# Kernel optimization log

Hardware: AMD Instinct MI355X
Metric: run time of the kernel (lower is better)

The kernel has to match this reference:

```python
import jax, jax.numpy as jnp
import numpy as np

NUM_POINTS = 500_000
DIM = 3
WINDOW = 64  # 4**DIM cubic B-spline stencil
INV_CELL = 20.0
ORIGIN = (0.0, 0.0, 0.0)


def setup_inputs() -> dict:
    key = jax.random.key(0)
    # particle positions in the interior of the unit cube
    position_stack = jax.random.uniform(
        key, (NUM_POINTS, DIM), dtype=jnp.float32, minval=0.1, maxval=0.9
    )
    return {"position_stack": position_stack}


def _middle_splines(x, h):
    """Cubic B-spline basis and gradient ('middle_splines' branch; the source's
    lax.switch uses index=0 unconditionally). x = dist in grid units, shape [...]."""
    c1 = (x >= -2) & (x < -1)
    c2 = (x >= -1) & (x < 0)
    c3 = (x >= 0) & (x < 1)
    c4 = (x >= 1) & (x < 2)
    basis = jnp.select(
        [c1, c2, c3, c4],
        [
            ((1.0 / 6.0 * x + 1.0) * x + 2.0) * x + 4.0 / 3.0,
            (-0.5 * x - 1.0) * x * x + 2.0 / 3.0,
            (0.5 * x - 1.0) * x * x + 2.0 / 3.0,
            ((-1.0 / 6.0 * x + 1.0) * x - 2.0) * x + 4.0 / 3.0,
        ],
        0.0,
    )
    dbasis = jnp.select(
        [c1, c2, c3, c4],
        [
            h * ((0.5 * x + 2.0) * x + 2.0),
            h * (-1.5 * x - 2.0) * x,
            h * (1.5 * x - 2.0) * x,
            h * ((-0.5 * x + 2.0) * x - 2.0),
        ],
        0.0,
    )
    return basis, dbasis


def _forward(position_stack):
    origin = jnp.asarray(ORIGIN, dtype=position_stack.dtype)
    rel = (position_stack - origin) * INV_CELL            # [N, 3] in grid units
    base = jnp.floor(rel) - 1.0                           # lower corner of 4^3 stencil
    ar = jnp.arange(4, dtype=position_stack.dtype)
    offs = jnp.stack(jnp.meshgrid(ar, ar, ar, indexing="ij"), axis=-1).reshape(-1, DIM)  # [64, 3]
    dist = rel[:, None, :] - (base[:, None, :] + offs[None, :, :])  # [N, 64, 3], in [-2, 2)
    b, db = _middle_splines(dist, INV_CELL)
    shapef_stack = jnp.prod(b, axis=-1)                   # [N, 64]
    shapef_grad_stack = jnp.stack(
        [
            db[..., 0] * b[..., 1] * b[..., 2],
            db[..., 1] * b[..., 0] * b[..., 2],
            db[..., 2] * b[..., 0] * b[..., 1],
        ],
        axis=-1,
    )                                                     # [N, 64, 3]
    return shapef_stack, shapef_grad_stack


def reference(position_stack):
    return _forward(position_stack)
```

## Files before the change

### kernel.cpp

```cpp
#include <hip/hip_runtime.h>

#ifndef INV_CELL_H
#define INV_CELL_H 20.0f
#endif

__device__ __forceinline__ void spline_eval(float f, float g, int idx,
                                            float& b, float& db) {
    float u  = (idx & 1) ? f : g;
    float u2 = u * u;
    float u3 = u2 * u;
    bool outer = (idx == 0) || (idx == 3);
    float b_out = u3 * (1.0f / 6.0f);
    float b_in  = fmaf(0.5f, u3, fmaf(-1.0f, u2, 2.0f / 3.0f));
    b = outer ? b_out : b_in;
    float m_out = 0.5f * u2;
    float m_in  = u * fmaf(-1.5f, u, 2.0f);
    float mag = outer ? m_out : m_in;
    float sgn = (idx >= 2) ? INV_CELL_H : -INV_CELL_H;
    db = mag * sgn;
}

struct F3 { float x, y, z; };

__global__ void __launch_bounds__(256)
cubic_shapefn_kernel(const float* __restrict__ pos,
                     float* __restrict__ shapef,
                     float* __restrict__ grad,
                     int N) {
    int wave = blockIdx.x * 4 + (threadIdx.x >> 6);
    if (wave >= N) return;
    int lane = threadIdx.x & 63;

    float px = pos[(size_t)wave * 3 + 0];
    float py = pos[(size_t)wave * 3 + 1];
    float pz = pos[(size_t)wave * 3 + 2];

    float rx = px * INV_CELL_H, ry = py * INV_CELL_H, rz = pz * INV_CELL_H;
    float fx = rx - floorf(rx), fy = ry - floorf(ry), fz = rz - floorf(rz);
    float gx = 1.0f - fx,       gy = 1.0f - fy,       gz = 1.0f - fz;

    int i = (lane >> 4) & 3;
    int j = (lane >> 2) & 3;
    int k = lane & 3;

    float bx, dbx, by, dby, bz, dbz;
    spline_eval(fx, gx, i, bx, dbx);
    spline_eval(fy, gy, j, by, dby);
    spline_eval(fz, gz, k, bz, dbz);

    float pyz = by * bz;
    float s   = bx * pyz;
    float gxv = dbx * pyz;
    float gyv = dby * (bx * bz);
    float gzv = dbz * (bx * by);

    shapef[(size_t)wave * 64 + lane] = s;

    F3 v{gxv, gyv, gzv};
    *(F3*)(grad + (size_t)wave * 192 + (size_t)lane * 3) = v;
}

extern "C" void kernel_launch(void* const* d_in, const int* in_sizes, int n_in,
                              void* d_out, int out_size, void* d_ws, size_t ws_size,
                              hipStream_t stream) {
    const float* pos = (const float*)d_in[0];
    int N = in_sizes[0] / 3;
    float* shapef = (float*)d_out;
    float* grad   = shapef + (size_t)N * 64;
    int blocks = (N + 3) / 4;
    cubic_shapefn_kernel<<<blocks, 256, 0, stream>>>(pos, shapef, grad, N);
}
```

Baseline: 536.4 us.

## Map 16 threads per point with vectorized nontemporal stores and grid-stride loop

Each point is now handled by 16 threads instead of 64. Each thread computes four z-stencil entries and writes them with 128-bit nontemporal stores instead of scalar and 12-byte stores. The launch becomes a persistent grid-stride loop capped at 2048 blocks, with occupancy hints in launch_bounds. This targets the write-bandwidth-bound output, reducing store instruction count and cache pollution, at the cost of more registers and less parallelism per point.

```diff
diff --git a/kernel.cpp b/kernel.cpp
--- a/kernel.cpp
+++ b/kernel.cpp
@@ -3,6 +3,8 @@
 #ifndef INV_CELL_H
 #define INV_CELL_H 20.0f
 #endif
+
+typedef float f32x4 __attribute__((ext_vector_type(4)));
 
 __device__ __forceinline__ void spline_eval(float f, float g, int idx,
                                             float& b, float& db) {
@@ -20,44 +22,57 @@
     db = mag * sgn;
 }
 
-struct F3 { float x, y, z; };
-
-__global__ void __launch_bounds__(256)
+__global__ void __launch_bounds__(256, 8)
 cubic_shapefn_kernel(const float* __restrict__ pos,
                      float* __restrict__ shapef,
                      float* __restrict__ grad,
                      int N) {
-    int wave = blockIdx.x * 4 + (threadIdx.x >> 6);
-    if (wave >= N) return;
-    int lane = threadIdx.x & 63;
+    const int t = threadIdx.x & 15;
+    const int i = t >> 2;
+    const int j = t & 3;
+    const int group0  = (int)((blockIdx.x * blockDim.x + threadIdx.x) >> 4);
+    const int ngroups = (int)((gridDim.x * blockDim.x) >> 4);
 
-    float px = pos[(size_t)wave * 3 + 0];
-    float py = pos[(size_t)wave * 3 + 1];
-    float pz = pos[(size_t)wave * 3 + 2];
+    for (int p = group0; p < N; p += ngroups) {
+        float px = pos[(size_t)p * 3 + 0];
+        float py = pos[(size_t)p * 3 + 1];
+        float pz = pos[(size_t)p * 3 + 2];
 
-    float rx = px * INV_CELL_H, ry = py * INV_CELL_H, rz = pz * INV_CELL_H;
-    float fx = rx - floorf(rx), fy = ry - floorf(ry), fz = rz - floorf(rz);
-    float gx = 1.0f - fx,       gy = 1.0f - fy,       gz = 1.0f - fz;
+        float rx = px * INV_CELL_H, ry = py * INV_CELL_H, rz = pz * INV_CELL_H;
+        float fx = rx - floorf(rx), fy = ry - floorf(ry), fz = rz - floorf(rz);
+        float gx = 1.0f - fx,       gy = 1.0f - fy,       gz = 1.0f - fz;
 
-    int i = (lane >> 4) & 3;
-    int j = (lane >> 2) & 3;
-    int k = lane & 3;
+        float bx, dbx, by, dby;
+        spline_eval(fx, gx, i, bx, dbx);
+        spline_eval(fy, gy, j, by, dby);
 
-    float bx, dbx, by, dby, bz, dbz;
-    spline_eval(fx, gx, i, bx, dbx);
-    spline_eval(fy, gy, j, by, dby);
-    spline_eval(fz, gz, k, bz, dbz);
+        float bz[4], dbz[4];
+#pragma unroll
+        for (int k = 0; k < 4; ++k) spline_eval(fz, gz, k, bz[k], dbz[k]);
 
-    float pyz = by * bz;
-    float s   = bx * pyz;
-    float gxv = dbx * pyz;
-    float gyv = dby * (bx * bz);
-    float gzv = dbz * (bx * by);
+        float A  = bx * by;
+        float Bx = dbx * by;
+        float By = bx * dby;
 
-    shapef[(size_t)wave * 64 + lane] = s;
+        f32x4 sv = { A * bz[0], A * bz[1], A * bz[2], A * bz[3] };
 
-    F3 v{gxv, gyv, gzv};
-    *(F3*)(grad + (size_t)wave * 192 + (size_t)lane * 3) = v;
+        float gxk[4], gyk[4], gzk[4];
+#pragma unroll
+        for (int k = 0; k < 4; ++k) {
+            gxk[k] = Bx * bz[k];
+            gyk[k] = By * bz[k];
+            gzk[k] = A  * dbz[k];
+        }
+        f32x4 q0 = { gxk[0], gyk[0], gzk[0], gxk[1] };
+        f32x4 q1 = { gyk[1], gzk[1], gxk[2], gyk[2] };
+        f32x4 q2 = { gzk[2], gxk[3], gyk[3], gzk[3] };
+
+        __builtin_nontemporal_store(sv, (f32x4*)(shapef + (size_t)p * 64 + t * 4));
+        float* gbase = grad + (size_t)p * 192 + t * 12;
+        __builtin_nontemporal_store(q0, (f32x4*)(gbase + 0));
+        __builtin_nontemporal_store(q1, (f32x4*)(gbase + 4));
+        __builtin_nontemporal_store(q2, (f32x4*)(gbase + 8));
+    }
 }
 
 extern "C" void kernel_launch(void* const* d_in, const int* in_sizes, int n_in,
@@ -67,6 +82,8 @@
     int N = in_sizes[0] / 3;
     float* shapef = (float*)d_out;
     float* grad   = shapef + (size_t)N * 64;
-    int blocks = (N + 3) / 4;
+    int needed = (N + 15) / 16;
+    int blocks = 2048;
+    if (blocks > needed) blocks = needed;
     cubic_shapefn_kernel<<<blocks, 256, 0, stream>>>(pos, shapef, grad, N);
 }
```

After: 671.2 us. +25.1%, slower.
